# Performance work log

Measured on AMD Instinct MI355X. Metric: run time of the kernel, lower is better.

## Reference

```python
import jax
import jax.numpy as jnp
import numpy as np

L, H_DIM = 8192, 128
ATTN_WINDOW, STRIDE = 3, 2


def setup_inputs() -> dict:
    key = jax.random.key(0)
    k1, k2, k3, k4, k5 = jax.random.split(key, 5)
    input_sequence = jax.random.normal(k1, (L, H_DIM), dtype=jnp.float32)
    # zoh-discretized diagonal decays exp(Lambda*Delta) lie in (0,1)
    Lambda_bar = jax.random.uniform(k2, (H_DIM, H_DIM), dtype=jnp.float32,
                                    minval=0.5, maxval=0.999)
    C_tilde = jax.random.normal(k3, (H_DIM, H_DIM), dtype=jnp.float32) / jnp.sqrt(
        jnp.float32(H_DIM))
    w_q = jax.random.normal(k4, (ATTN_WINDOW, ATTN_WINDOW), dtype=jnp.float32) * 0.1
    D = jax.random.normal(k5, (ATTN_WINDOW,), dtype=jnp.float32)
    return {
        "input_sequence": input_sequence,
        "Lambda_bar": Lambda_bar,
        "C_tilde": C_tilde,
        "w_q": w_q,
        "D": D,
        "attn_window": ATTN_WINDOW,
        "stride": STRIDE,
    }


def reference(input_sequence, Lambda_bar, C_tilde, w_q, D, attn_window, stride):
    # input_sequence: (L, H); Lambda_bar, C_tilde: (H, H); w_q: (W, W); D: (W,)
    Lseq, H = input_sequence.shape
    num_windows = (Lseq - attn_window) // stride + 1
    idx = jnp.arange(num_windows)[:, None] * stride + jnp.arange(attn_window)
    windows = input_sequence[idx]  # (T, W, H)

    # local self-attention per window: x.T @ w_q @ x  -> (T, H, H), axes (t, a, d)
    lsa = jnp.einsum("twa,wv,tvd->tad", windows, w_q, windows)

    # diagonal linear SSM scan over windows, vectorized over both H axes:
    # carry[a, d] = Lambda_bar[a, d] * carry[a, d] + lsa[t, a, d]
    def step(carry, inp):
        carry = Lambda_bar * carry + inp
        return carry, carry

    init = jnp.zeros((H, H), dtype=input_sequence.dtype)
    _, zs = jax.lax.scan(step, init, lsa)  # (T, a, d)

    # original stacks per-d scans on axis=1 giving (T, d, a), then C_tilde @ u
    # contracts d: out[t, h, a] = sum_d C_tilde[h, d] * zs[t, a, d]
    zs_out = jnp.einsum("hd,tad->tha", C_tilde, zs)  # (T, H, H)

    # os = vmap(u.T @ D): (T, H)
    os = jnp.einsum("twh,w->th", windows, D)
    return zs_out, os
```

## Files before the change

### kernel.cpp

```cpp
#include <hip/hip_runtime.h>

#define L_   8192
#define H_   128
#define T_   4095
#define CH_  16
#define NC_  256

typedef __bf16 bf16x8 __attribute__((ext_vector_type(8)));
typedef unsigned short ushort8 __attribute__((ext_vector_type(8)));
typedef float f32x4 __attribute__((ext_vector_type(4)));

__device__ __forceinline__ unsigned short f2bf(float f) {
    unsigned int u = __builtin_bit_cast(unsigned int, f);
    u += 0x7fffu + ((u >> 16) & 1u);
    return (unsigned short)(u >> 16);
}

__global__ __launch_bounds__(256) void pass1_kernel(const float* __restrict__ X,
                                                    const float* __restrict__ Lam,
                                                    const float* __restrict__ wq,
                                                    float* __restrict__ ebuf) {
    __shared__ float y_s[3][128];
    __shared__ float xa_s[3][32];

    const int tid = threadIdx.x;
    const int c   = blockIdx.x;
    const int a0  = blockIdx.y * 32;
    const int a_l = tid & 31;
    const int dg  = tid >> 5;

    float z[16], lam[16];
    {
        const float* lp = Lam + (size_t)(a0 + a_l) * H_ + dg * 16;
        #pragma unroll
        for (int j = 0; j < 16; ++j) { lam[j] = lp[j]; z[j] = 0.f; }
    }
    const float w00 = wq[0], w01 = wq[1], w02 = wq[2];
    const float w10 = wq[3], w11 = wq[4], w12 = wq[5];
    const float w20 = wq[6], w21 = wq[7], w22 = wq[8];

    const int t0 = c * CH_;
    const int t1 = min(t0 + CH_, T_);

    for (int t = t0; t < t1; ++t) {
        __syncthreads();
        const float* xr = X + (size_t)(2 * t) * H_;
        if (tid < 128) {
            float xd0 = xr[tid], xd1 = xr[H_ + tid], xd2 = xr[2 * H_ + tid];
            y_s[0][tid] = w00 * xd0 + w01 * xd1 + w02 * xd2;
            y_s[1][tid] = w10 * xd0 + w11 * xd1 + w12 * xd2;
            y_s[2][tid] = w20 * xd0 + w21 * xd1 + w22 * xd2;
        } else if (tid < 224) {
            int li = tid - 128;
            xa_s[li >> 5][li & 31] = xr[(li >> 5) * H_ + a0 + (li & 31)];
        }
        __syncthreads();
        const float xa0 = xa_s[0][a_l], xa1 = xa_s[1][a_l], xa2 = xa_s[2][a_l];
        #pragma unroll
        for (int j = 0; j < 16; ++j) {
            const int d = dg * 16 + j;
            float u = xa0 * y_s[0][d] + xa1 * y_s[1][d] + xa2 * y_s[2][d];
            z[j] = fmaf(lam[j], z[j], u);
        }
    }
    float* ep = ebuf + (size_t)c * (H_ * H_) + (size_t)(a0 + a_l) * H_ + dg * 16;
    #pragma unroll
    for (int j = 0; j < 16; ++j) ep[j] = z[j];
}

__global__ __launch_bounds__(256) void pass2_kernel(const float* __restrict__ Lam,
                                                    float* __restrict__ ebuf) {
    const int entry = blockIdx.x * 256 + threadIdx.x;
    const float lam = Lam[entry];
    float p = lam * lam; p = p * p; p = p * p; p = p * p;
    float z = 0.f;
    for (int cb = 0; cb < NC_; cb += 8) {
        float tmp[8];
        #pragma unroll
        for (int i = 0; i < 8; ++i)
            tmp[i] = ebuf[(size_t)(cb + i) * (H_ * H_) + entry];
        #pragma unroll
        for (int i = 0; i < 8; ++i) {
            ebuf[(size_t)(cb + i) * (H_ * H_) + entry] = z;
            z = fmaf(p, z, tmp[i]);
        }
    }
}

__global__ __launch_bounds__(256) void pass3_kernel(const float* __restrict__ X,
                                                    const float* __restrict__ Lam,
                                                    const float* __restrict__ Cm,
                                                    const float* __restrict__ wq,
                                                    const float* __restrict__ Dv,
                                                    const float* __restrict__ carry,
                                                    float* __restrict__ out,
                                                    float* __restrict__ os) {
    __shared__ unsigned short z_s[32][136];
    __shared__ float y_s[3][128];
    __shared__ float xa_s[3][32];

    const int tid  = threadIdx.x;
    const int c    = blockIdx.x;
    const int a0   = blockIdx.y * 32;
    const int lane = tid & 63;
    const int wave = tid >> 6;
    const int m    = lane & 15;
    const int q    = lane >> 4;

    ushort8 cfrag[2][4];
    #pragma unroll
    for (int ni = 0; ni < 2; ++ni) {
        const int h = (wave * 2 + ni) * 16 + m;
        #pragma unroll
        for (int kt = 0; kt < 4; ++kt) {
            const float* src = Cm + h * H_ + kt * 32 + q * 8;
            ushort8 v;
            #pragma unroll
            for (int j = 0; j < 8; ++j) v[j] = f2bf(src[j]);
            cfrag[ni][kt] = v;
        }
    }

    const int a_l = tid & 31;
    const int dg  = tid >> 5;
    float z[16], lam[16];
    {
        const float* lp = Lam   + (size_t)(a0 + a_l) * H_ + dg * 16;
        const float* cp = carry + (size_t)c * (H_ * H_) + (size_t)(a0 + a_l) * H_ + dg * 16;
        #pragma unroll
        for (int j = 0; j < 16; ++j) { lam[j] = lp[j]; z[j] = cp[j]; }
    }
    const float w00 = wq[0], w01 = wq[1], w02 = wq[2];
    const float w10 = wq[3], w11 = wq[4], w12 = wq[5];
    const float w20 = wq[6], w21 = wq[7], w22 = wq[8];
    const float d0 = Dv[0], d1 = Dv[1], d2 = Dv[2];
    const bool do_os = (blockIdx.y == 0);

    const int t0 = c * CH_;
    const int t1 = min(t0 + CH_, T_);

    for (int t = t0; t < t1; ++t) {
        __syncthreads();
        const float* xr = X + (size_t)(2 * t) * H_;
        if (tid < 128) {
            float xd0 = xr[tid], xd1 = xr[H_ + tid], xd2 = xr[2 * H_ + tid];
            y_s[0][tid] = w00 * xd0 + w01 * xd1 + w02 * xd2;
            y_s[1][tid] = w10 * xd0 + w11 * xd1 + w12 * xd2;
            y_s[2][tid] = w20 * xd0 + w21 * xd1 + w22 * xd2;
            if (do_os) os[t * H_ + tid] = d0 * xd0 + d1 * xd1 + d2 * xd2;
        } else if (tid < 224) {
            int li = tid - 128;
            xa_s[li >> 5][li & 31] = xr[(li >> 5) * H_ + a0 + (li & 31)];
        }
        __syncthreads();

        {
            const float xa0 = xa_s[0][a_l], xa1 = xa_s[1][a_l], xa2 = xa_s[2][a_l];
            #pragma unroll
            for (int j = 0; j < 16; ++j) {
                const int d = dg * 16 + j;
                float u = xa0 * y_s[0][d] + xa1 * y_s[1][d] + xa2 * y_s[2][d];
                z[j] = fmaf(lam[j], z[j], u);
            }
            ushort8 zb0, zb1;
            #pragma unroll
            for (int j = 0; j < 8; ++j) { zb0[j] = f2bf(z[j]); zb1[j] = f2bf(z[j + 8]); }
            *(ushort8*)&z_s[a_l][dg * 16]     = zb0;
            *(ushort8*)&z_s[a_l][dg * 16 + 8] = zb1;
        }
        __syncthreads();

        f32x4 acc[2][2] = {};
        #pragma unroll
        for (int kt = 0; kt < 4; ++kt) {
            bf16x8 za = __builtin_bit_cast(bf16x8, *(const ushort8*)&z_s[m][kt * 32 + q * 8]);
            bf16x8 zb = __builtin_bit_cast(bf16x8, *(const ushort8*)&z_s[16 + m][kt * 32 + q * 8]);
            #pragma unroll
            for (int ni = 0; ni < 2; ++ni) {
                bf16x8 cf = __builtin_bit_cast(bf16x8, cfrag[ni][kt]);
                acc[0][ni] = __builtin_amdgcn_mfma_f32_16x16x32_bf16(za, cf, acc[0][ni], 0, 0, 0);
                acc[1][ni] = __builtin_amdgcn_mfma_f32_16x16x32_bf16(zb, cf, acc[1][ni], 0, 0, 0);
            }
        }
        float* ob = out + (size_t)t * (H_ * H_) + a0;
        #pragma unroll
        for (int mi = 0; mi < 2; ++mi) {
            #pragma unroll
            for (int ni = 0; ni < 2; ++ni) {
                const int h = (wave * 2 + ni) * 16 + m;
                *(f32x4*)&ob[(size_t)h * H_ + mi * 16 + q * 4] = acc[mi][ni];
            }
        }
    }
}

extern "C" void kernel_launch(void* const* d_in, const int* in_sizes, int n_in,
                              void* d_out, int out_size, void* d_ws, size_t ws_size,
                              hipStream_t stream) {
    const float* X   = (const float*)d_in[0];
    const float* Lam = (const float*)d_in[1];
    const float* Cm  = (const float*)d_in[2];
    const float* wq  = (const float*)d_in[3];
    const float* Dv  = (const float*)d_in[4];
    float* out = (float*)d_out;
    float* os  = out + (size_t)T_ * H_ * H_;
    float* ebuf = (float*)d_ws;

    pass1_kernel<<<dim3(NC_, 4), 256, 0, stream>>>(X, Lam, wq, ebuf);
    pass2_kernel<<<64, 256, 0, stream>>>(Lam, ebuf);
    pass3_kernel<<<dim3(NC_, 4), 256, 0, stream>>>(X, Lam, Cm, wq, Dv, ebuf, out, os);
}
```

Measured before the change: 346.6 us.

## Store local scan states in output, then fix up carries and project in place

The first pass now writes every per-step local scan state straight into the output buffer, using double-buffered shared staging and prefetching of the next rows. The carry pass reads chunk-final states from that buffer. A new per-timestep pass applies the carry correction via lambda powers and runs the C projection with MFMA in place, rewriting each output slab. This removes the recomputation of the scan in the last pass but adds a full write and read round trip of the large output tensor.

```diff
diff --git a/kernel.cpp b/kernel.cpp
--- a/kernel.cpp
+++ b/kernel.cpp
@@ -8,6 +8,7 @@
 
 typedef __bf16 bf16x8 __attribute__((ext_vector_type(8)));
 typedef unsigned short ushort8 __attribute__((ext_vector_type(8)));
+typedef unsigned short us4 __attribute__((ext_vector_type(4)));
 typedef float f32x4 __attribute__((ext_vector_type(4)));
 
 __device__ __forceinline__ unsigned short f2bf(float f) {
@@ -16,96 +17,171 @@
     return (unsigned short)(u >> 16);
 }
 
-__global__ __launch_bounds__(256) void pass1_kernel(const float* __restrict__ X,
+__device__ __forceinline__ float powe(float l, int e) {
+    float r = (e & 1) ? l : 1.f;
+    float b = l * l;
+    if (e & 2) r *= b;
+    b *= b;
+    if (e & 4) r *= b;
+    b *= b;
+    if (e & 8) r *= b;
+    if (e & 16) r = b * b;
+    return r;
+}
+
+__global__ __launch_bounds__(256) void passA_kernel(const float* __restrict__ X,
                                                     const float* __restrict__ Lam,
                                                     const float* __restrict__ wq,
-                                                    float* __restrict__ ebuf) {
-    __shared__ float y_s[3][128];
-    __shared__ float xa_s[3][32];
+                                                    const float* __restrict__ Dv,
+                                                    float* __restrict__ out,
+                                                    float* __restrict__ os) {
+    __shared__ float y_s[2][3][128];
+    __shared__ float xa_s[2][3][16];
 
     const int tid = threadIdx.x;
     const int c   = blockIdx.x;
-    const int a0  = blockIdx.y * 32;
-    const int a_l = tid & 31;
-    const int dg  = tid >> 5;
-
-    float z[16], lam[16];
+    const int a0  = blockIdx.y * 16;
+    const int a_l = tid >> 4;
+    const int dg  = tid & 15;
+    const int d0  = dg * 8;
+
+    float z[8], lam[8];
     {
-        const float* lp = Lam + (size_t)(a0 + a_l) * H_ + dg * 16;
-        #pragma unroll
-        for (int j = 0; j < 16; ++j) { lam[j] = lp[j]; z[j] = 0.f; }
+        const float* lp = Lam + (size_t)(a0 + a_l) * H_ + d0;
+        #pragma unroll
+        for (int j = 0; j < 8; ++j) { lam[j] = lp[j]; z[j] = 0.f; }
     }
     const float w00 = wq[0], w01 = wq[1], w02 = wq[2];
     const float w10 = wq[3], w11 = wq[4], w12 = wq[5];
     const float w20 = wq[6], w21 = wq[7], w22 = wq[8];
-
-    const int t0 = c * CH_;
-    const int t1 = min(t0 + CH_, T_);
-
+    const float dv0 = Dv[0], dv1 = Dv[1], dv2 = Dv[2];
+
+    const bool ystage = tid < 128;
+    const bool astage = (tid >= 128) && (tid < 176);
+    const bool do_os  = (blockIdx.y == 0) && ystage;
+    const int  wA = (tid - 128) >> 4, aA = (tid - 128) & 15;
+
+    const int t0 = c * CH_, t1 = min(t0 + CH_, T_);
+
+    float xd0 = 0.f, xd1 = 0.f, xd2 = 0.f, xav = 0.f;
+    {
+        const float* xr = X + (size_t)(2 * t0) * H_;
+        if (ystage)      { xd0 = xr[tid]; xd1 = xr[H_ + tid]; xd2 = xr[2 * H_ + tid]; }
+        else if (astage) { xav = xr[wA * H_ + a0 + aA]; }
+    }
+    if (ystage) {
+        const int sw = (4 * tid) ^ ((tid & 32) >> 1);
+        char* yb0 = (char*)&y_s[0][0][0];
+        *(float*)(yb0 + sw)        = w00 * xd0 + w01 * xd1 + w02 * xd2;
+        *(float*)(yb0 + 512 + sw)  = w10 * xd0 + w11 * xd1 + w12 * xd2;
+        *(float*)(yb0 + 1024 + sw) = w20 * xd0 + w21 * xd1 + w22 * xd2;
+        if (do_os) os[(size_t)t0 * H_ + tid] = dv0 * xd0 + dv1 * xd1 + dv2 * xd2;
+    } else if (astage) {
+        xa_s[0][wA][aA] = xav;
+    }
+    __syncthreads();
+
+    int p = 0;
     for (int t = t0; t < t1; ++t) {
+        const bool more = (t + 1 < t1);
+        if (more) {
+            const float* xr = X + (size_t)(2 * (t + 1)) * H_;
+            if (ystage)      { xd0 = xr[tid]; xd1 = xr[H_ + tid]; xd2 = xr[2 * H_ + tid]; }
+            else if (astage) { xav = xr[wA * H_ + a0 + aA]; }
+        }
+        const float xa0 = xa_s[p][0][a_l], xa1 = xa_s[p][1][a_l], xa2 = xa_s[p][2][a_l];
+        const char* yb = (const char*)y_s + p * 1536;
+        const int s4 = (dg & 4) << 2;
+        const int lo = (32 * dg) ^ s4;
+        const int hi = (32 * dg + 16) ^ s4;
+        f32x4 yl0 = *(const f32x4*)(yb + lo),        yh0 = *(const f32x4*)(yb + hi);
+        f32x4 yl1 = *(const f32x4*)(yb + 512 + lo),  yh1 = *(const f32x4*)(yb + 512 + hi);
+        f32x4 yl2 = *(const f32x4*)(yb + 1024 + lo), yh2 = *(const f32x4*)(yb + 1024 + hi);
+        #pragma unroll
+        for (int j = 0; j < 4; ++j) {
+            float u  = xa0 * yl0[j] + xa1 * yl1[j] + xa2 * yl2[j];
+            z[j]     = fmaf(lam[j], z[j], u);
+            float u2 = xa0 * yh0[j] + xa1 * yh1[j] + xa2 * yh2[j];
+            z[j + 4] = fmaf(lam[j + 4], z[j + 4], u2);
+        }
+        float* op = out + (size_t)t * (H_ * H_) + (size_t)(a0 + a_l) * H_ + d0;
+        f32x4 zlo = {z[0], z[1], z[2], z[3]};
+        f32x4 zhi = {z[4], z[5], z[6], z[7]};
+        *(f32x4*)op       = zlo;
+        *(f32x4*)(op + 4) = zhi;
+        if (more) {
+            if (ystage) {
+                const int sw = (4 * tid) ^ ((tid & 32) >> 1);
+                char* ybn = (char*)y_s + (p ^ 1) * 1536;
+                *(float*)(ybn + sw)        = w00 * xd0 + w01 * xd1 + w02 * xd2;
+                *(float*)(ybn + 512 + sw)  = w10 * xd0 + w11 * xd1 + w12 * xd2;
+                *(float*)(ybn + 1024 + sw) = w20 * xd0 + w21 * xd1 + w22 * xd2;
+                if (do_os) os[(size_t)(t + 1) * H_ + tid] = dv0 * xd0 + dv1 * xd1 + dv2 * xd2;
+            } else if (astage) {
+                xa_s[p ^ 1][wA][aA] = xav;
+            }
+        }
         __syncthreads();
-        const float* xr = X + (size_t)(2 * t) * H_;
-        if (tid < 128) {
-            float xd0 = xr[tid], xd1 = xr[H_ + tid], xd2 = xr[2 * H_ + tid];
-            y_s[0][tid] = w00 * xd0 + w01 * xd1 + w02 * xd2;
-            y_s[1][tid] = w10 * xd0 + w11 * xd1 + w12 * xd2;
-            y_s[2][tid] = w20 * xd0 + w21 * xd1 + w22 * xd2;
-        } else if (tid < 224) {
-            int li = tid - 128;
-            xa_s[li >> 5][li & 31] = xr[(li >> 5) * H_ + a0 + (li & 31)];
-        }
-        __syncthreads();
-        const float xa0 = xa_s[0][a_l], xa1 = xa_s[1][a_l], xa2 = xa_s[2][a_l];
-        #pragma unroll
-        for (int j = 0; j < 16; ++j) {
-            const int d = dg * 16 + j;
-            float u = xa0 * y_s[0][d] + xa1 * y_s[1][d] + xa2 * y_s[2][d];
-            z[j] = fmaf(lam[j], z[j], u);
-        }
-    }
-    float* ep = ebuf + (size_t)c * (H_ * H_) + (size_t)(a0 + a_l) * H_ + dg * 16;
-    #pragma unroll
-    for (int j = 0; j < 16; ++j) ep[j] = z[j];
+        p ^= 1;
+    }
 }
 
 __global__ __launch_bounds__(256) void pass2_kernel(const float* __restrict__ Lam,
-                                                    float* __restrict__ ebuf) {
-    const int entry = blockIdx.x * 256 + threadIdx.x;
-    const float lam = Lam[entry];
-    float p = lam * lam; p = p * p; p = p * p; p = p * p;
+                                                    const float* __restrict__ zsl,
+                                                    float* __restrict__ carry) {
+    const int e = blockIdx.x * 256 + threadIdx.x;
+    const float lam = Lam[e];
+    float l2 = lam * lam, l4 = l2 * l2, l8 = l4 * l4;
+    const float l16 = l8 * l8;
     float z = 0.f;
     for (int cb = 0; cb < NC_; cb += 8) {
         float tmp[8];
         #pragma unroll
-        for (int i = 0; i < 8; ++i)
-            tmp[i] = ebuf[(size_t)(cb + i) * (H_ * H_) + entry];
-        #pragma unroll
         for (int i = 0; i < 8; ++i) {
-            ebuf[(size_t)(cb + i) * (H_ * H_) + entry] = z;
-            z = fmaf(p, z, tmp[i]);
-        }
-    }
-}
-
-__global__ __launch_bounds__(256) void pass3_kernel(const float* __restrict__ X,
-                                                    const float* __restrict__ Lam,
+            const int cc = cb + i;
+            tmp[i] = (cc < NC_ - 1)
+                   ? zsl[(size_t)(cc * CH_ + CH_ - 1) * (H_ * H_) + e] : 0.f;
+        }
+        #pragma unroll
+        for (int i = 0; i < 8; ++i) {
+            carry[(size_t)(cb + i) * (H_ * H_) + e] = z;
+            z = fmaf(l16, z, tmp[i]);
+        }
+    }
+}
+
+__global__ __launch_bounds__(256) void passC_kernel(const float* __restrict__ Lam,
                                                     const float* __restrict__ Cm,
-                                                    const float* __restrict__ wq,
-                                                    const float* __restrict__ Dv,
                                                     const float* __restrict__ carry,
-                                                    float* __restrict__ out,
-                                                    float* __restrict__ os) {
-    __shared__ unsigned short z_s[32][136];
-    __shared__ float y_s[3][128];
-    __shared__ float xa_s[3][32];
-
-    const int tid  = threadIdx.x;
-    const int c    = blockIdx.x;
-    const int a0   = blockIdx.y * 32;
-    const int lane = tid & 63;
-    const int wave = tid >> 6;
-    const int m    = lane & 15;
-    const int q    = lane >> 4;
+                                                    float* __restrict__ out) {
+    __shared__ unsigned short zs[H_ * H_];
+
+    const int t   = blockIdx.x;
+    const int c   = t >> 4;
+    const int e   = (t & 15) + 1;
+    const int tid = threadIdx.x;
+    const int lane = tid & 63, wave = tid >> 6;
+    const int m = lane & 15, q = lane >> 4;
+
+    const size_t tb = (size_t)t << 14;
+    const float* zp = out   + tb + (size_t)tid * 4;
+    const float* cp = carry + ((size_t)c << 14) + (size_t)tid * 4;
+    const float* lp = Lam   + (size_t)tid * 4;
+    const int r0   = tid >> 5;
+    const int colb = (tid & 31) * 8;
+    #pragma unroll
+    for (int i = 0; i < 16; ++i) {
+        const int off = i * 1024;
+        f32x4 zv = *(const f32x4*)(zp + off);
+        f32x4 cv = *(const f32x4*)(cp + off);
+        f32x4 lv = *(const f32x4*)(lp + off);
+        us4 zb;
+        #pragma unroll
+        for (int j = 0; j < 4; ++j)
+            zb[j] = f2bf(fmaf(powe(lv[j], e), cv[j], zv[j]));
+        const int a = i * 8 + r0;
+        *(us4*)((char*)zs + a * 256 + (colb ^ ((a & 15) << 4))) = zb;
+    }
 
     ushort8 cfrag[2][4];
     #pragma unroll
@@ -114,82 +190,36 @@
         #pragma unroll
         for (int kt = 0; kt < 4; ++kt) {
             const float* src = Cm + h * H_ + kt * 32 + q * 8;
+            f32x4 c0 = *(const f32x4*)src;
+            f32x4 c1 = *(const f32x4*)(src + 4);
             ushort8 v;
             #pragma unroll
-            for (int j = 0; j < 8; ++j) v[j] = f2bf(src[j]);
+            for (int j = 0; j < 4; ++j) { v[j] = f2bf(c0[j]); v[j + 4] = f2bf(c1[j]); }
             cfrag[ni][kt] = v;
         }
     }
-
-    const int a_l = tid & 31;
-    const int dg  = tid >> 5;
-    float z[16], lam[16];
-    {
-        const float* lp = Lam   + (size_t)(a0 + a_l) * H_ + dg * 16;
-        const float* cp = carry + (size_t)c * (H_ * H_) + (size_t)(a0 + a_l) * H_ + dg * 16;
-        #pragma unroll
-        for (int j = 0; j < 16; ++j) { lam[j] = lp[j]; z[j] = cp[j]; }
-    }
-    const float w00 = wq[0], w01 = wq[1], w02 = wq[2];
-    const float w10 = wq[3], w11 = wq[4], w12 = wq[5];
-    const float w20 = wq[6], w21 = wq[7], w22 = wq[8];
-    const float d0 = Dv[0], d1 = Dv[1], d2 = Dv[2];
-    const bool do_os = (blockIdx.y == 0);
-
-    const int t0 = c * CH_;
-    const int t1 = min(t0 + CH_, T_);
-
-    for (int t = t0; t < t1; ++t) {
-        __syncthreads();
-        const float* xr = X + (size_t)(2 * t) * H_;
-        if (tid < 128) {
-            float xd0 = xr[tid], xd1 = xr[H_ + tid], xd2 = xr[2 * H_ + tid];
-            y_s[0][tid] = w00 * xd0 + w01 * xd1 + w02 * xd2;
-            y_s[1][tid] = w10 * xd0 + w11 * xd1 + w12 * xd2;
-            y_s[2][tid] = w20 * xd0 + w21 * xd1 + w22 * xd2;
-            if (do_os) os[t * H_ + tid] = d0 * xd0 + d1 * xd1 + d2 * xd2;
-        } else if (tid < 224) {
-            int li = tid - 128;
-            xa_s[li >> 5][li & 31] = xr[(li >> 5) * H_ + a0 + (li & 31)];
-        }
-        __syncthreads();
-
-        {
-            const float xa0 = xa_s[0][a_l], xa1 = xa_s[1][a_l], xa2 = xa_s[2][a_l];
+    __syncthreads();
+
+    f32x4 acc[8][2] = {};
+    #pragma unroll
+    for (int kt = 0; kt < 4; ++kt) {
+        const int cb = (64 * kt + 16 * q) ^ (m << 4);
+        #pragma unroll
+        for (int mi = 0; mi < 8; ++mi) {
+            bf16x8 za = *(const bf16x8*)((char*)zs + (mi * 16 + m) * 256 + cb);
             #pragma unroll
-            for (int j = 0; j < 16; ++j) {
-                const int d = dg * 16 + j;
-                float u = xa0 * y_s[0][d] + xa1 * y_s[1][d] + xa2 * y_s[2][d];
-                z[j] = fmaf(lam[j], z[j], u);
-            }
-            ushort8 zb0, zb1;
-            #pragma unroll
-            for (int j = 0; j < 8; ++j) { zb0[j] = f2bf(z[j]); zb1[j] = f2bf(z[j + 8]); }
-            *(ushort8*)&z_s[a_l][dg * 16]     = zb0;
-            *(ushort8*)&z_s[a_l][dg * 16 + 8] = zb1;
-        }
-        __syncthreads();
-
-        f32x4 acc[2][2] = {};
-        #pragma unroll
-        for (int kt = 0; kt < 4; ++kt) {
-            bf16x8 za = __builtin_bit_cast(bf16x8, *(const ushort8*)&z_s[m][kt * 32 + q * 8]);
-            bf16x8 zb = __builtin_bit_cast(bf16x8, *(const ushort8*)&z_s[16 + m][kt * 32 + q * 8]);
-            #pragma unroll
-            for (int ni = 0; ni < 2; ++ni) {
-                bf16x8 cf = __builtin_bit_cast(bf16x8, cfrag[ni][kt]);
-                acc[0][ni] = __builtin_amdgcn_mfma_f32_16x16x32_bf16(za, cf, acc[0][ni], 0, 0, 0);
-                acc[1][ni] = __builtin_amdgcn_mfma_f32_16x16x32_bf16(zb, cf, acc[1][ni], 0, 0, 0);
-            }
-        }
-        float* ob = out + (size_t)t * (H_ * H_) + a0;
-        #pragma unroll
-        for (int mi = 0; mi < 2; ++mi) {
-            #pragma unroll
-            for (int ni = 0; ni < 2; ++ni) {
-                const int h = (wave * 2 + ni) * 16 + m;
-                *(f32x4*)&ob[(size_t)h * H_ + mi * 16 + q * 4] = acc[mi][ni];
-            }
+            for (int ni = 0; ni < 2; ++ni)
+                acc[mi][ni] = __builtin_amdgcn_mfma_f32_16x16x32_bf16(
+                    za, __builtin_bit_cast(bf16x8, cfrag[ni][kt]), acc[mi][ni], 0, 0, 0);
+        }
+    }
+    float* ob = out + tb;
+    #pragma unroll
+    for (int mi = 0; mi < 8; ++mi) {
+        #pragma unroll
+        for (int ni = 0; ni < 2; ++ni) {
+            const int h = (wave * 2 + ni) * 16 + m;
+            *(f32x4*)&ob[(size_t)h * H_ + mi * 16 + q * 4] = acc[mi][ni];
         }
     }
 }
@@ -204,9 +234,9 @@
     const float* Dv  = (const float*)d_in[4];
     float* out = (float*)d_out;
     float* os  = out + (size_t)T_ * H_ * H_;
-    float* ebuf = (float*)d_ws;
-
-    pass1_kernel<<<dim3(NC_, 4), 256, 0, stream>>>(X, Lam, wq, ebuf);
-    pass2_kernel<<<64, 256, 0, stream>>>(Lam, ebuf);
-    pass3_kernel<<<dim3(NC_, 4), 256, 0, stream>>>(X, Lam, Cm, wq, Dv, ebuf, out, os);
-}
+    float* cry = (float*)d_ws;
+
+    passA_kernel<<<dim3(NC_, 8), 256, 0, stream>>>(X, Lam, wq, Dv, out, os);
+    pass2_kernel<<<64, 256, 0, stream>>>(Lam, out, cry);
+    passC_kernel<<<T_, 256, 0, stream>>>(Lam, Cm, cry, out);
+}
```

After: 485.6 us. 40.1% more time.
